# Kernel tuning notes

Hardware: AMD Instinct MI355X
Metric: run time of the kernel (lower is better)

Reference implementation:

```python
import jax, jax.numpy as jnp
import numpy as np

V, E, S, B, T = 100000, 64, 4, 2048, 200
D = 2 * E          # memory_vector_dim
C = E              # controller_units
CIN = 2 * E + D    # controller input: x_t (2E) + prev read (D)
P = 2 * (D + 1) + 2 * D  # (key+beta) for read & write heads + erase + add


def setup_inputs() -> dict:
    key = jax.random.key(0)
    ks = jax.random.split(key, 16)
    g = lambda k, sh, sc=0.05: jax.random.normal(k, sh, dtype=jnp.float32) * sc
    return {
        "item": jax.random.randint(ks[0], (B,), 0, V),
        "cate": jax.random.randint(ks[1], (B,), 0, V),
        "hist_item": jax.random.randint(ks[2], (B, T), 0, V),
        "hist_cate": jax.random.randint(ks[3], (B, T), 0, V),
        "mask": jnp.ones((B, T), jnp.float32),
        "embedding": g(ks[4], (V, E)),
        "gru_Wih": g(ks[5], (3 * C, CIN)),
        "gru_Whh": g(ks[6], (3 * C, C)),
        "gru_bih": jnp.zeros((3 * C,), jnp.float32),
        "gru_bhh": jnp.zeros((3 * C,), jnp.float32),
        "Wp": g(ks[7], (P, C)),
        "bp": jnp.zeros((P,), jnp.float32),
        "Wo": g(ks[8], (E, C + D)),
        "bo": jnp.zeros((E,), jnp.float32),
        "M0": g(ks[9], (S, D), 0.1),
        "fc1_w": g(ks[10], (200, 5 * E)),
        "fc1_b": jnp.zeros((200,), jnp.float32),
        "prelu1_a": jnp.full((1,), 0.25, jnp.float32),
        "fc2_w": g(ks[11], (80, 200)),
        "fc2_b": jnp.zeros((80,), jnp.float32),
        "prelu2_a": jnp.full((1,), 0.25, jnp.float32),
        "fc3_w": g(ks[12], (2, 80)),
        "fc3_b": jnp.zeros((2,), jnp.float32),
    }


def _cos_addr(k, beta, M):
    # content addressing: softmax(beta * cosine_sim(k, M))  k:[B,D] M:[B,S,D]
    kn = k / (jnp.linalg.norm(k, axis=-1, keepdims=True) + 1e-8)
    Mn = M / (jnp.linalg.norm(M, axis=-1, keepdims=True) + 1e-8)
    K = jnp.einsum('bd,bsd->bs', kn, Mn)
    return jax.nn.softmax(beta[:, None] * K, axis=-1)


def _prelu(x, a):
    return jnp.where(x > 0, x, a * x)


def _mimn_rnn(hist_emb, mask, gru_Wih, gru_Whh, gru_bih, gru_bhh, Wp, bp, Wo, bo, M0):
    Bn = hist_emb.shape[0]
    h0 = jnp.zeros((Bn, C), hist_emb.dtype)
    r0 = jnp.zeros((Bn, D), hist_emb.dtype)
    Mi = jnp.broadcast_to(M0[None], (Bn, S, D))

    def step(carry, inp):
        h, M, read = carry
        x_t, m_t = inp                      # x_t [B,2E], m_t [B]
        ctrl_in = jnp.concatenate([x_t, read], axis=-1)
        gi = ctrl_in @ gru_Wih.T + gru_bih
        gh = h @ gru_Whh.T + gru_bhh
        i_r, i_z, i_n = jnp.split(gi, 3, axis=-1)
        h_r, h_z, h_n = jnp.split(gh, 3, axis=-1)
        rg = jax.nn.sigmoid(i_r + h_r)
        zg = jax.nn.sigmoid(i_z + h_z)
        ng = jnp.tanh(i_n + rg * h_n)
        h_new = (1.0 - zg) * ng + zg * h
        # head parameters
        p = h_new @ Wp.T + bp               # [B, P]
        hp_r, hp_w = p[:, :D + 1], p[:, D + 1:2 * (D + 1)]
        erase = jax.nn.sigmoid(p[:, 2 * (D + 1):2 * (D + 1) + D])
        add = jnp.tanh(p[:, -D:])
        k_r, beta_r = jnp.tanh(hp_r[:, :D]), jax.nn.softplus(hp_r[:, D])
        k_w, beta_w = jnp.tanh(hp_w[:, :D]), jax.nn.softplus(hp_w[:, D])
        w_r = _cos_addr(k_r, beta_r, M)
        w_w = _cos_addr(k_w, beta_w, M)
        read_new = jnp.einsum('bs,bsd->bd', w_r, M)
        M_new = M * (1.0 - w_w[..., None] * erase[:, None, :]) + w_w[..., None] * add[:, None, :]
        out = jnp.concatenate([h_new, read_new], axis=-1) @ Wo.T + bo  # [B,E]
        # sequence-length masking (dynamic_rnn semantics)
        v = (m_t > 0)[:, None]
        h = jnp.where(v, h_new, h)
        read = jnp.where(v, read_new, read)
        M = jnp.where(v[..., None], M_new, M)
        out = jnp.where(v, out, jnp.zeros_like(out))
        return (h, M, read), out

    xs = (jnp.swapaxes(hist_emb, 0, 1), jnp.swapaxes(mask, 0, 1))  # [T,B,...]
    _, outs = jax.lax.scan(step, (h0, Mi, r0), xs)
    return jnp.swapaxes(outs, 0, 1)  # [B,T,E]


def reference(item, cate, hist_item, hist_cate, mask, embedding,
              gru_Wih, gru_Whh, gru_bih, gru_bhh, Wp, bp, Wo, bo, M0,
              fc1_w, fc1_b, prelu1_a, fc2_w, fc2_b, prelu2_a, fc3_w, fc3_b):
    item_emb = jnp.concatenate([embedding[item], embedding[cate]], axis=1)      # [B,2E]
    hist_emb = jnp.concatenate([embedding[hist_item], embedding[hist_cate]], axis=2)  # [B,T,2E]
    seq_len = mask.sum(1).astype(jnp.int32)
    outputs = _mimn_rnn(hist_emb, mask, gru_Wih, gru_Whh, gru_bih, gru_bhh, Wp, bp, Wo, bo, M0)
    last_out = jnp.take_along_axis(outputs, (seq_len - 1)[:, None, None], axis=1)[:, 0, :]
    hist_sum = (hist_emb * mask[..., None]).sum(1)                              # [B,2E]
    x = jnp.concatenate([item_emb, hist_sum, last_out], axis=1)                 # [B,5E]
    x = _prelu(x @ fc1_w.T + fc1_b, prelu1_a)
    x = _prelu(x @ fc2_w.T + fc2_b, prelu2_a)
    return x @ fc3_w.T + fc3_b
```

## Files before the change

kernel.cpp:

```cpp
#include <hip/hip_runtime.h>

#define VV 100000
#define BB 2048
#define TT 200
#define GG 192
#define PP 514
#define RPB 8
#define NBT 1563

typedef _Float16 half8 __attribute__((ext_vector_type(8)));
typedef float floatx4 __attribute__((ext_vector_type(4)));
#define MFMA16(a, b, c) __builtin_amdgcn_mfma_f32_16x16x32_f16((a), (b), (c), 0, 0, 0)

#define BARRIER_LDS() do { \
    __asm__ volatile("s_waitcnt lgkmcnt(0)" ::: "memory"); \
    __builtin_amdgcn_s_barrier(); } while (0)

__device__ __forceinline__ float fsigm(float x) { return 1.0f / (1.0f + __expf(-x)); }
__device__ __forceinline__ float ftanh(float x) {
    float e = __expf(2.0f * x);
    return 1.0f - 2.0f / (e + 1.0f);
}
__device__ __forceinline__ float fsoftplus(float x) {
    float e = __expf(-fabsf(x));
    return fmaxf(x, 0.0f) + __logf(1.0f + e);
}

#define DPP_ADD(x, ctrl, rmask) \
    ((x) + __int_as_float(__builtin_amdgcn_update_dpp( \
        0, __float_as_int(x), (ctrl), (rmask), 0xf, true)))
__device__ __forceinline__ float wsum64(float x) {
    x = DPP_ADD(x, 0x111, 0xf);
    x = DPP_ADD(x, 0x112, 0xf);
    x = DPP_ADD(x, 0x114, 0xf);
    x = DPP_ADD(x, 0x118, 0xf);
    x = DPP_ADD(x, 0x142, 0xa);
    x = DPP_ADD(x, 0x143, 0xc);
    return __int_as_float(__builtin_amdgcn_readlane(__float_as_int(x), 63));
}
__device__ __forceinline__ float dot4(float4 w, float4 a) {
    return w.x * a.x + w.y * a.y + w.z * a.z + w.w * a.w;
}

__global__ __launch_bounds__(256) void prep(
    const float* __restrict__ emb,
    const float* __restrict__ Wih,
    const float* __restrict__ bih,
    const int* __restrict__ hist_item, const int* __restrict__ hist_cate,
    const float* __restrict__ mask,
    float* __restrict__ GIi, float* __restrict__ GIc,
    float* __restrict__ hist_sum, int* __restrict__ seqlen)
{
    __shared__ __align__(16) _Float16 sE16[64 * 72];
    const int tid = threadIdx.x;
    const int wv = tid >> 6, lane = tid & 63;
    const int nlo = lane & 15, kg = lane >> 4;

    if (blockIdx.x < NBT) {
        const int v0 = blockIdx.x * 64;
        for (int i = tid; i < 64 * 64; i += 256) {
            int vv = i >> 6, k = i & 63;
            int gv = v0 + vv;
            sE16[vv * 72 + k] = (gv < VV) ? (_Float16)emb[(size_t)gv * 64 + k]
                                          : (_Float16)0.f;
        }
        half8 WF[6][2];
        float bias[6];
#pragma unroll
        for (int j = 0; j < 6; ++j) {
            int pid = 6 * wv + j;
            int tb = pid / 12, nt = pid % 12;
            int n = nt * 16 + nlo;
#pragma unroll
            for (int kb = 0; kb < 2; ++kb) {
                half8 f;
#pragma unroll
                for (int q = 0; q < 8; ++q)
                    f[q] = (_Float16)Wih[n * 256 + tb * 64 + kb * 32 + kg * 8 + q];
                WF[j][kb] = f;
            }
            bias[j] = tb ? 0.f : bih[n];
        }
        __syncthreads();
#pragma unroll
        for (int mt = 0; mt < 4; ++mt) {
            const int ar = (16 * mt + nlo) * 72 + 8 * kg;
            half8 a0 = *(const half8*)&sE16[ar];
            half8 a1 = *(const half8*)&sE16[ar + 32];
#pragma unroll
            for (int j = 0; j < 6; ++j) {
                floatx4 acc = {0.f, 0.f, 0.f, 0.f};
                acc = MFMA16(a0, WF[j][0], acc);
                acc = MFMA16(a1, WF[j][1], acc);
                int pid = 6 * wv + j;
                int tb = pid / 12, nt = pid % 12;
                float* dst = tb ? GIc : GIi;
                int n = nt * 16 + nlo;
#pragma unroll
                for (int q = 0; q < 4; ++q) {
                    int gv = v0 + 16 * mt + 4 * kg + q;
                    if (gv < VV) dst[(size_t)gv * GG + n] = acc[q] + bias[j];
                }
            }
        }
    } else {
        const int hb = blockIdx.x - NBT;
        const int b = hb * 2 + (wv >> 1);
        const int* hidx = (wv & 1) ? hist_cate : hist_item;
        float acc = 0.f;
        for (int t = 0; t < TT; ++t) {
            float m = mask[(size_t)b * TT + t];
            int idx = hidx[(size_t)b * TT + t];
            acc += m * emb[(size_t)idx * 64 + lane];
        }
        hist_sum[(size_t)b * 128 + (wv & 1) * 64 + lane] = acc;
        if ((wv & 1) == 0) {
            float s = 0.f;
            for (int t = lane; t < TT; t += 64) s += mask[(size_t)b * TT + t];
            s = wsum64(s);
            if (lane == 0) seqlen[b] = (int)(s + 0.5f);
        }
    }
}

__global__ __attribute__((amdgpu_flat_work_group_size(512, 512))) void mimn_rnn(
    const int* __restrict__ hist_item, const int* __restrict__ hist_cate,
    const float* __restrict__ mask,
    const float* __restrict__ Wih,
    const float* __restrict__ Whh,
    const float* __restrict__ bhh,
    const float* __restrict__ Wp,
    const float* __restrict__ bp,
    const float* __restrict__ Wo,
    const float* __restrict__ bo,
    const float* __restrict__ M0,
    const float* __restrict__ GIi, const float* __restrict__ GIc,
    const int* __restrict__ seqlen,
    float* __restrict__ last_out)
{
    __shared__ __align__(16) float sU[4160];
    __shared__ __align__(16) _Float16 act16[16 * 200];
    __shared__ __align__(16) _Float16 hn16[16 * 72];
    __shared__ float sHnF[RPB * 64];
    __shared__ float sWpT[2 * 64];
    __shared__ unsigned char sMaskB[RPB * TT];

    const int tid = threadIdx.x;
    const int b0 = blockIdx.x * RPB;
    const int wv = tid >> 6, lane = tid & 63;
    const int nlo = lane & 15, kg = lane >> 4;
    const bool hasN = wv >= 4;

    for (int i = tid; i < 16 * 200; i += 512) act16[i] = (_Float16)0.f;
    for (int i = tid; i < 16 * 72; i += 512) hn16[i] = (_Float16)0.f;
    for (int i = tid; i < RPB * 64; i += 512) sHnF[i] = 0.f;
    if (tid < 128) sWpT[tid] = Wp[512 * 64 + tid];
    for (int i = tid; i < RPB * TT; i += 512) {
        int r = i / TT, tt = i - r * TT;
        sMaskB[i] = (mask[(size_t)(b0 + r) * TT + tt] > 0.f) ? 1 : 0;
    }

    float hreg = 0.f;
    float M1[4], M2[4];
#pragma unroll
    for (int s = 0; s < 4; ++s) {
        M1[s] = M0[s * 128 + lane];
        M2[s] = M0[s * 128 + 64 + lane];
    }
    const float bhhRZ = bhh[16 * wv + nlo];
    const float bhhN  = hasN ? bhh[128 + 16 * (wv - 4) + nlo] : 0.f;
    float bpP[4];
#pragma unroll
    for (int i = 0; i < 4; ++i) bpP[i] = bp[16 * (wv + 8 * i) + nlo];
    const float bpT = (tid < 16) ? bp[512 + (tid >> 3)] : 0.f;

    half8 WG[6];
    {
        int n = 16 * wv + nlo;
#pragma unroll
        for (int kb = 0; kb < 6; ++kb) {
            half8 f;
#pragma unroll
            for (int j = 0; j < 8; ++j) {
                int k = 32 * kb + 8 * kg + j;
                float w = (k < 128) ? Wih[n * 256 + 128 + k] : Whh[n * 64 + (k - 128)];
                f[j] = (_Float16)w;
            }
            WG[kb] = f;
        }
    }
    half8 WN[6];
    if (hasN) {
        int n = 128 + 16 * (wv - 4) + nlo;
#pragma unroll
        for (int kb = 0; kb < 4; ++kb) {
            half8 f;
#pragma unroll
            for (int j = 0; j < 8; ++j) f[j] = (_Float16)Wih[n * 256 + 128 + 32 * kb + 8 * kg + j];
            WN[kb] = f;
        }
#pragma unroll
        for (int kb = 0; kb < 2; ++kb) {
            half8 f;
#pragma unroll
            for (int j = 0; j < 8; ++j) f[j] = (_Float16)Whh[n * 64 + 32 * kb + 8 * kg + j];
            WN[4 + kb] = f;
        }
    } else {
#pragma unroll
        for (int q = 0; q < 6; ++q) WN[q] = half8{};
    }
    half8 WP[8];
#pragma unroll
    for (int i = 0; i < 4; ++i) {
        int n = 16 * (wv + 8 * i) + nlo;
#pragma unroll
        for (int kb = 0; kb < 2; ++kb) {
            half8 f;
#pragma unroll
            for (int j = 0; j < 8; ++j) f[j] = (_Float16)Wp[n * 64 + 32 * kb + 8 * kg + j];
            WP[2 * i + kb] = f;
        }
    }

    int ts = seqlen[b0 + wv] - 1;
    ts = ts < 0 ? 0 : (ts > TT - 1 ? TT - 1 : ts);

    float giA, giB, giC, gcA, gcB, gcC;
    {
        int ri = hist_item[(size_t)(b0 + wv) * TT];
        int rc = hist_cate[(size_t)(b0 + wv) * TT];
        giA = GIi[(size_t)ri * GG + lane];
        giB = GIi[(size_t)ri * GG + 64 + lane];
        giC = GIi[(size_t)ri * GG + 128 + lane];
        gcA = GIc[(size_t)rc * GG + lane];
        gcB = GIc[(size_t)rc * GG + 64 + lane];
        gcC = GIc[(size_t)rc * GG + 128 + lane];
    }
    __syncthreads();

    for (int t = 0; t < TT; ++t) {
        {
            const int abase = nlo * 200 + 8 * kg;
            floatx4 accRZ = {0.f, 0.f, 0.f, 0.f};
            floatx4 accI = {0.f, 0.f, 0.f, 0.f};
            floatx4 accH = {0.f, 0.f, 0.f, 0.f};
            half8 a0 = *(const half8*)&act16[abase];
            half8 a1 = *(const half8*)&act16[abase + 32];
            half8 a2 = *(const half8*)&act16[abase + 64];
            accRZ = MFMA16(a0, WG[0], accRZ);
            accRZ = MFMA16(a1, WG[1], accRZ);
            accRZ = MFMA16(a2, WG[2], accRZ);
            if (hasN) {
                accI = MFMA16(a0, WN[0], accI);
                accI = MFMA16(a1, WN[1], accI);
                accI = MFMA16(a2, WN[2], accI);
            }
            a0 = *(const half8*)&act16[abase + 96];
            a1 = *(const half8*)&act16[abase + 128];
            a2 = *(const half8*)&act16[abase + 160];
            accRZ = MFMA16(a0, WG[3], accRZ);
            accRZ = MFMA16(a1, WG[4], accRZ);
            accRZ = MFMA16(a2, WG[5], accRZ);
            if (hasN) {
                accI = MFMA16(a0, WN[3], accI);
                accH = MFMA16(a1, WN[4], accH);
                accH = MFMA16(a2, WN[5], accH);
            }
            if (kg < 2) {
                int n = 16 * wv + nlo;
#pragma unroll
                for (int q = 0; q < 4; ++q) sU[(4 * kg + q) * 132 + n] = accRZ[q] + bhhRZ;
                if (hasN) {
                    int n64 = 16 * (wv - 4) + nlo;
#pragma unroll
                    for (int q = 0; q < 4; ++q) {
                        sU[1056 + (4 * kg + q) * 68 + n64] = accI[q];
                        sU[1600 + (4 * kg + q) * 68 + n64] = accH[q] + bhhN;
                    }
                }
            }
        }
        BARRIER_LDS();
        bool vld;
        {
            const int r = wv;
            float g_r = sU[r * 132 + lane] + giA + gcA;
            float g_z = sU[r * 132 + 64 + lane] + giB + gcB;
            float i_n = sU[1056 + r * 68 + lane] + giC + gcC;
            float h_n = sU[1600 + r * 68 + lane];
            float rg = fsigm(g_r);
            float zg = fsigm(g_z);
            float ng = ftanh(i_n + rg * h_n);
            float hn = (1.f - zg) * ng + zg * hreg;
            vld = sMaskB[r * TT + t] != 0;
            float hc = vld ? hn : hreg;
            hreg = hc;
            act16[r * 200 + 128 + lane] = (_Float16)hc;
            hn16[r * 72 + lane] = (_Float16)hn;
            sHnF[r * 64 + lane] = hn;
        }
        {
            int tn = (t + 1 < TT) ? t + 1 : TT - 1;
            int ri = hist_item[(size_t)(b0 + wv) * TT + tn];
            int rc = hist_cate[(size_t)(b0 + wv) * TT + tn];
            giA = GIi[(size_t)ri * GG + lane];
            giB = GIi[(size_t)ri * GG + 64 + lane];
            giC = GIi[(size_t)ri * GG + 128 + lane];
            gcA = GIc[(size_t)rc * GG + lane];
            gcB = GIc[(size_t)rc * GG + 64 + lane];
            gcC = GIc[(size_t)rc * GG + 128 + lane];
        }
        BARRIER_LDS();
        {
            const int bbase = nlo * 72 + 8 * kg;
            half8 b0f = *(const half8*)&hn16[bbase];
            half8 b1f = *(const half8*)&hn16[bbase + 32];
#pragma unroll
            for (int i = 0; i < 4; ++i) {
                floatx4 acc = {0.f, 0.f, 0.f, 0.f};
                acc = MFMA16(b0f, WP[2 * i], acc);
                acc = MFMA16(b1f, WP[2 * i + 1], acc);
                if (kg < 2) {
                    int n = 16 * (wv + 8 * i) + nlo;
#pragma unroll
                    for (int q = 0; q < 4; ++q) sU[(4 * kg + q) * 520 + n] = acc[q] + bpP[i];
                }
            }
        }
        if (tid < 16) {
            int r = tid & 7, j = tid >> 3;
            float acc = 0.f;
#pragma unroll
            for (int k = 0; k < 64; ++k) acc += sHnF[r * 64 + k] * sWpT[j * 64 + k];
            sU[r * 520 + 512 + j] = acc + bpT;
        }
        BARRIER_LDS();
        {
            const int row = wv;
            const int pb = row * 520;
#define PV(n) (sU[pb + (n)])
            float kr1 = ftanh(PV(lane)),       kr2 = ftanh(PV(64 + lane));
            float beta_r = fsoftplus(PV(128));
            float kw1 = ftanh(PV(129 + lane)), kw2 = ftanh(PV(193 + lane));
            float beta_w = fsoftplus(PV(257));
            float er1 = fsigm(PV(258 + lane)), er2 = fsigm(PV(322 + lane));
            float ad1 = ftanh(PV(386 + lane)), ad2 = ftanh(PV(450 + lane));
#undef PV
            float nkr = sqrtf(wsum64(kr1 * kr1 + kr2 * kr2)) + 1e-8f;
            float nkw = sqrtf(wsum64(kw1 * kw1 + kw2 * kw2)) + 1e-8f;
            float Kr[4], Kw[4];
#pragma unroll
            for (int s = 0; s < 4; ++s) {
                float nM = sqrtf(wsum64(M1[s] * M1[s] + M2[s] * M2[s])) + 1e-8f;
                float dr = wsum64(kr1 * M1[s] + kr2 * M2[s]);
                float dw = wsum64(kw1 * M1[s] + kw2 * M2[s]);
                Kr[s] = dr / (nkr * nM);
                Kw[s] = dw / (nkw * nM);
            }
            float wr_[4], ww_[4];
            {
                float mx = fmaxf(fmaxf(beta_r * Kr[0], beta_r * Kr[1]),
                                 fmaxf(beta_r * Kr[2], beta_r * Kr[3]));
                float sum = 0.f;
#pragma unroll
                for (int s = 0; s < 4; ++s) { wr_[s] = __expf(beta_r * Kr[s] - mx); sum += wr_[s]; }
                float inv = 1.f / sum;
#pragma unroll
                for (int s = 0; s < 4; ++s) wr_[s] *= inv;
            }
            {
                float mx = fmaxf(fmaxf(beta_w * Kw[0], beta_w * Kw[1]),
                                 fmaxf(beta_w * Kw[2], beta_w * Kw[3]));
                float sum = 0.f;
#pragma unroll
                for (int s = 0; s < 4; ++s) { ww_[s] = __expf(beta_w * Kw[s] - mx); sum += ww_[s]; }
                float inv = 1.f / sum;
#pragma unroll
                for (int s = 0; s < 4; ++s) ww_[s] *= inv;
            }
            float rn1 = 0.f, rn2 = 0.f;
#pragma unroll
            for (int s = 0; s < 4; ++s) { rn1 += wr_[s] * M1[s]; rn2 += wr_[s] * M2[s]; }
            if (vld) {
#pragma unroll
                for (int s = 0; s < 4; ++s) {
                    M1[s] = M1[s] * (1.f - ww_[s] * er1) + ww_[s] * ad1;
                    M2[s] = M2[s] * (1.f - ww_[s] * er2) + ww_[s] * ad2;
                }
                act16[row * 200 + lane]      = (_Float16)rn1;
                act16[row * 200 + 64 + lane] = (_Float16)rn2;
            }
            if (t == ts) {
                float* stash = &sU[pb];
                stash[lane] = rn1; stash[64 + lane] = rn2;
                __asm__ volatile("s_waitcnt lgkmcnt(0)" ::: "memory");
                float acc = bo[lane];
                const float* wo = Wo + lane * GG;
                for (int k = 0; k < 64; ++k)  acc += sHnF[row * 64 + k] * wo[k];
                for (int k = 0; k < 128; ++k) acc += stash[k] * wo[64 + k];
                if (!vld) acc = 0.f;
                last_out[(size_t)(b0 + row) * 64 + lane] = acc;
            }
        }
        BARRIER_LDS();
    }
}

__global__ __launch_bounds__(128) void final_mlp(
    const int* __restrict__ item, const int* __restrict__ cate,
    const float* __restrict__ emb,
    const float* __restrict__ hist_sum, const float* __restrict__ last_out,
    const float* __restrict__ fc1w, const float* __restrict__ fc1b,
    const float* __restrict__ pa1,
    const float* __restrict__ fc2w, const float* __restrict__ fc2b,
    const float* __restrict__ pa2,
    const float* __restrict__ fc3w, const float* __restrict__ fc3b,
    float* __restrict__ out)
{
    __shared__ float sX[320], sH1[200], sH2[80];
    int b = blockIdx.x, tid = threadIdx.x;
    int it = item[b], ct = cate[b];
    for (int i = tid; i < 320; i += 128) {
        float val;
        if (i < 64)       val = emb[(size_t)it * 64 + i];
        else if (i < 128) val = emb[(size_t)ct * 64 + (i - 64)];
        else if (i < 256) val = hist_sum[(size_t)b * 128 + (i - 128)];
        else              val = last_out[(size_t)b * 64 + (i - 256)];
        sX[i] = val;
    }
    __syncthreads();
    float a1 = pa1[0];
    for (int o = tid; o < 200; o += 128) {
        const float4* w = (const float4*)(fc1w + o * 320);
        float acc = fc1b[o];
#pragma unroll
        for (int q = 0; q < 80; ++q) acc += dot4(w[q], *(const float4*)&sX[q * 4]);
        sH1[o] = acc > 0.f ? acc : a1 * acc;
    }
    __syncthreads();
    float a2 = pa2[0];
    for (int o = tid; o < 80; o += 128) {
        const float4* w = (const float4*)(fc2w + o * 200);
        float acc = fc2b[o];
#pragma unroll
        for (int q = 0; q < 50; ++q) acc += dot4(w[q], *(const float4*)&sH1[q * 4]);
        sH2[o] = acc > 0.f ? acc : a2 * acc;
    }
    __syncthreads();
    if (tid < 2) {
        const float4* w = (const float4*)(fc3w + tid * 80);
        float acc = fc3b[tid];
#pragma unroll
        for (int q = 0; q < 20; ++q) acc += dot4(w[q], *(const float4*)&sH2[q * 4]);
        out[b * 2 + tid] = acc;
    }
}

extern "C" void kernel_launch(void* const* d_in, const int* in_sizes, int n_in,
                              void* d_out, int out_size, void* d_ws, size_t ws_size,
                              hipStream_t stream) {
    (void)in_sizes; (void)n_in; (void)out_size; (void)ws_size;
    const int*   item      = (const int*)d_in[0];
    const int*   cate      = (const int*)d_in[1];
    const int*   hist_item = (const int*)d_in[2];
    const int*   hist_cate = (const int*)d_in[3];
    const float* mask = (const float*)d_in[4];
    const float* emb  = (const float*)d_in[5];
    const float* Wih  = (const float*)d_in[6];
    const float* Whh  = (const float*)d_in[7];
    const float* bih  = (const float*)d_in[8];
    const float* bhh  = (const float*)d_in[9];
    const float* Wp   = (const float*)d_in[10];
    const float* bp   = (const float*)d_in[11];
    const float* Wo   = (const float*)d_in[12];
    const float* bo   = (const float*)d_in[13];
    const float* M0   = (const float*)d_in[14];
    const float* fc1w = (const float*)d_in[15];
    const float* fc1b = (const float*)d_in[16];
    const float* pa1  = (const float*)d_in[17];
    const float* fc2w = (const float*)d_in[18];
    const float* fc2b = (const float*)d_in[19];
    const float* pa2  = (const float*)d_in[20];
    const float* fc3w = (const float*)d_in[21];
    const float* fc3b = (const float*)d_in[22];

    float* GIi = (float*)d_ws;
    float* GIc = GIi + (size_t)VV * GG;
    float* hist_sum = GIc + (size_t)VV * GG;
    float* last_out = hist_sum + (size_t)BB * 128;
    int* seqlen = (int*)(last_out + (size_t)BB * 64);

    prep<<<NBT + BB / 2, 256, 0, stream>>>(emb, Wih, bih, hist_item, hist_cate,
                                           mask, GIi, GIc, hist_sum, seqlen);
    mimn_rnn<<<BB / RPB, 512, 0, stream>>>(hist_item, hist_cate, mask, Wih, Whh, bhh,
                                           Wp, bp, Wo, bo, M0, GIi, GIc, seqlen, last_out);
    final_mlp<<<BB, 128, 0, stream>>>(item, cate, emb, hist_sum, last_out,
                                      fc1w, fc1b, pa1, fc2w, fc2b, pa2, fc3w, fc3b,
                                      (float*)d_out);
}
```

Before: 1.069 ms.

## Defer write-head memory update into next step's MFMA phase

The write-head addressing and erase/add memory update are moved off the serial critical section after the projection. They now run at the start of the next timestep, interleaved with the GRU MFMA work. The raw projection values and memory norms are carried across steps in registers. This is meant to shorten the per-step dependent chain between barriers, at the cost of more live registers. The final memory update after the last step is skipped, but that update is never read.

```diff
diff --git a/kernel.cpp b/kernel.cpp
--- a/kernel.cpp
+++ b/kernel.cpp
@@ -237,6 +237,10 @@
         gcB = GIc[(size_t)rc * GG + 64 + lane];
         gcC = GIc[(size_t)rc * GG + 128 + lane];
     }
+    float pKw1 = 0.f, pKw2 = 0.f, pBw = 0.f, pEr1 = 0.f, pEr2 = 0.f;
+    float pAd1 = 0.f, pAd2 = 0.f;
+    float nMs[4] = {1.f, 1.f, 1.f, 1.f};
+    bool vldPrev = false;
     __syncthreads();
 
     for (int t = 0; t < TT; ++t) {
@@ -266,6 +270,34 @@
                 accI = MFMA16(a0, WN[3], accI);
                 accH = MFMA16(a1, WN[4], accH);
                 accH = MFMA16(a2, WN[5], accH);
+            }
+            if (t > 0) {
+                float kw1 = ftanh(pKw1), kw2 = ftanh(pKw2);
+                float beta_w = fsoftplus(pBw);
+                float nkw = sqrtf(wsum64(kw1 * kw1 + kw2 * kw2)) + 1e-8f;
+                float Kw[4];
+#pragma unroll
+                for (int s = 0; s < 4; ++s) {
+                    float dw = wsum64(kw1 * M1[s] + kw2 * M2[s]);
+                    Kw[s] = dw / (nkw * nMs[s]);
+                }
+                float ww_[4];
+                float mx = fmaxf(fmaxf(beta_w * Kw[0], beta_w * Kw[1]),
+                                 fmaxf(beta_w * Kw[2], beta_w * Kw[3]));
+                float sum = 0.f;
+#pragma unroll
+                for (int s = 0; s < 4; ++s) { ww_[s] = __expf(beta_w * Kw[s] - mx); sum += ww_[s]; }
+                float inv = 1.f / sum;
+                if (vldPrev) {
+                    float er1 = fsigm(pEr1), er2 = fsigm(pEr2);
+                    float ad1 = ftanh(pAd1), ad2 = ftanh(pAd2);
+#pragma unroll
+                    for (int s = 0; s < 4; ++s) {
+                        float w = ww_[s] * inv;
+                        M1[s] = M1[s] * (1.f - w * er1) + w * ad1;
+                        M2[s] = M2[s] * (1.f - w * er2) + w * ad2;
+                    }
+                }
             }
             if (kg < 2) {
                 int n = 16 * wv + nlo;
@@ -342,23 +374,20 @@
 #define PV(n) (sU[pb + (n)])
             float kr1 = ftanh(PV(lane)),       kr2 = ftanh(PV(64 + lane));
             float beta_r = fsoftplus(PV(128));
-            float kw1 = ftanh(PV(129 + lane)), kw2 = ftanh(PV(193 + lane));
-            float beta_w = fsoftplus(PV(257));
-            float er1 = fsigm(PV(258 + lane)), er2 = fsigm(PV(322 + lane));
-            float ad1 = ftanh(PV(386 + lane)), ad2 = ftanh(PV(450 + lane));
+            pKw1 = PV(129 + lane); pKw2 = PV(193 + lane);
+            pBw  = PV(257);
+            pEr1 = PV(258 + lane); pEr2 = PV(322 + lane);
+            pAd1 = PV(386 + lane); pAd2 = PV(450 + lane);
 #undef PV
             float nkr = sqrtf(wsum64(kr1 * kr1 + kr2 * kr2)) + 1e-8f;
-            float nkw = sqrtf(wsum64(kw1 * kw1 + kw2 * kw2)) + 1e-8f;
-            float Kr[4], Kw[4];
+            float Kr[4];
 #pragma unroll
             for (int s = 0; s < 4; ++s) {
-                float nM = sqrtf(wsum64(M1[s] * M1[s] + M2[s] * M2[s])) + 1e-8f;
+                nMs[s] = sqrtf(wsum64(M1[s] * M1[s] + M2[s] * M2[s])) + 1e-8f;
                 float dr = wsum64(kr1 * M1[s] + kr2 * M2[s]);
-                float dw = wsum64(kw1 * M1[s] + kw2 * M2[s]);
-                Kr[s] = dr / (nkr * nM);
-                Kw[s] = dw / (nkw * nM);
-            }
-            float wr_[4], ww_[4];
+                Kr[s] = dr / (nkr * nMs[s]);
+            }
+            float wr_[4];
             {
                 float mx = fmaxf(fmaxf(beta_r * Kr[0], beta_r * Kr[1]),
                                  fmaxf(beta_r * Kr[2], beta_r * Kr[3]));
@@ -369,25 +398,11 @@
 #pragma unroll
                 for (int s = 0; s < 4; ++s) wr_[s] *= inv;
             }
-            {
-                float mx = fmaxf(fmaxf(beta_w * Kw[0], beta_w * Kw[1]),
-                                 fmaxf(beta_w * Kw[2], beta_w * Kw[3]));
-                float sum = 0.f;
-#pragma unroll
-                for (int s = 0; s < 4; ++s) { ww_[s] = __expf(beta_w * Kw[s] - mx); sum += ww_[s]; }
-                float inv = 1.f / sum;
-#pragma unroll
-                for (int s = 0; s < 4; ++s) ww_[s] *= inv;
-            }
             float rn1 = 0.f, rn2 = 0.f;
 #pragma unroll
             for (int s = 0; s < 4; ++s) { rn1 += wr_[s] * M1[s]; rn2 += wr_[s] * M2[s]; }
+            vldPrev = vld;
             if (vld) {
-#pragma unroll
-                for (int s = 0; s < 4; ++s) {
-                    M1[s] = M1[s] * (1.f - ww_[s] * er1) + ww_[s] * ad1;
-                    M2[s] = M2[s] * (1.f - ww_[s] * er2) + ww_[s] * ad2;
-                }
                 act16[row * 200 + lane]      = (_Float16)rn1;
                 act16[row * 200 + 64 + lane] = (_Float16)rn2;
             }
```

Result: no change. 1.060 ms (-0.8%).
